# Performance work log

Hardware: AMD Instinct MI355X
Metric: run time of the kernel (lower is better)

The kernel has to match this reference:

```python
import jax, jax.numpy as jnp
import numpy as np

N = 20000      # nodes
E = 200000     # edges
F_IN = 512     # num_features
H = 1024       # hidden (hard-coded in module)
OUT = 128      # output_size


def setup_inputs() -> dict:
    key = jax.random.key(0)
    ks = jax.random.split(key, 12)
    x = jax.random.normal(ks[0], (N, F_IN), jnp.float32)
    edge_index = jax.random.randint(ks[1], (2, E), 0, N, dtype=jnp.int32)
    edge_weight = jax.random.uniform(ks[2], (E,), jnp.float32)
    # GCNConv weights (glorot-ish) and biases
    w1 = jax.random.normal(ks[3], (F_IN, H), jnp.float32) / np.sqrt(F_IN)
    b1 = jnp.zeros((H,), jnp.float32)
    w2 = jax.random.normal(ks[4], (H, OUT), jnp.float32) / np.sqrt(H)
    b2 = jnp.zeros((OUT,), jnp.float32)
    # residual Linear layers
    rw1 = jax.random.normal(ks[5], (F_IN, H), jnp.float32) / np.sqrt(F_IN)
    rb1 = jax.random.normal(ks[6], (H,), jnp.float32) * 0.01
    rw2 = jax.random.normal(ks[7], (H, OUT), jnp.float32) / np.sqrt(H)
    rb2 = jax.random.normal(ks[8], (OUT,), jnp.float32) * 0.01
    return {"x": x, "w1": w1, "b1": b1, "w2": w2, "b2": b2,
            "rw1": rw1, "rb1": rb1, "rw2": rw2, "rb2": rb2,
            "edge_weight": edge_weight, "edge_index": edge_index}


def gcn_conv(x, W, b, edge_index, edge_weight, n):
    """PyG GCNConv: linear transform, add self-loops (weight 1), sym-normalized scatter-add."""
    xw = x @ W                                             # [n, d_out]
    loop = jnp.arange(n, dtype=edge_index.dtype)
    row = jnp.concatenate([edge_index[0], loop])           # sources (x_j)
    col = jnp.concatenate([edge_index[1], loop])           # targets (aggregate here)
    ew = jnp.concatenate([edge_weight, jnp.ones((n,), xw.dtype)])
    deg = jax.ops.segment_sum(ew, col, num_segments=n)     # weighted in-degree
    dis = jnp.where(deg > 0, jax.lax.rsqrt(jnp.where(deg > 0, deg, 1.0)), 0.0)
    norm = dis[row] * ew * dis[col]                        # [E+n]
    msg = xw[row] * norm[:, None]                          # gather + scale
    out = jax.ops.segment_sum(msg, col, num_segments=n)    # scatter-add
    return out + b


def reference(x, w1, b1, w2, b2, rw1, rb1, rw2, rb2, edge_weight, edge_index):
    n = x.shape[0]
    h = jax.nn.relu(gcn_conv(x, w1, b1, edge_index, edge_weight, n) + (x @ rw1 + rb1))
    # F.dropout(training=False) is identity in eval mode
    out = gcn_conv(h, w2, b2, edge_index, edge_weight, n) + (h @ rw2 + rb2)
    return out
```

## Files before the change

kernel.cpp:

```cpp
#include <hip/hip_runtime.h>
#include <hip/hip_bf16.h>

#define NN 20000
#define EE 200000
#define FIN 512
#define HID 1024
#define OUTF 128
#define MPAD 20096

typedef unsigned short ush;
typedef __attribute__((ext_vector_type(8))) short bf16x8;
typedef __attribute__((ext_vector_type(4))) float f32x4;

__device__ __forceinline__ ush f2bf_rne(float f) {
    union { float f; unsigned u; } a; a.f = f;
    unsigned u = a.u;
    return (ush)((u + 0x7fffu + ((u >> 16) & 1u)) >> 16);
}
__device__ __forceinline__ float bf2f(ush h) {
    union { float f; unsigned u; } a; a.u = ((unsigned)h) << 16;
    return a.f;
}
__device__ __forceinline__ void split_bf(float v, ush& hi, ush& lo) {
    hi = f2bf_rne(v);
    lo = f2bf_rne(v - bf2f(hi));
}

__device__ __forceinline__ void gl16(const void* g, void* l) {
    __builtin_amdgcn_global_load_lds(
        (const __attribute__((address_space(1))) unsigned*)g,
        (__attribute__((address_space(3))) unsigned*)l, 16, 0, 0);
}

__global__ void init_kernel(float* deg, int* cnt, int n) {
    int i = blockIdx.x * blockDim.x + threadIdx.x;
    if (i < n) { deg[i] = 1.0f; cnt[i] = 0; }
}

__global__ void deg_count_kernel(const int* __restrict__ ei, const float* __restrict__ ew,
                                 float* deg, int* cnt, int e) {
    int idx = blockIdx.x * blockDim.x + threadIdx.x;
    if (idx < e) {
        int c = ei[EE + idx];
        atomicAdd(&deg[c], ew[idx]);
        atomicAdd(&cnt[c], 1);
    }
}

__global__ void dis_kernel(const float* __restrict__ deg, float* dis, int n) {
    int i = blockIdx.x * blockDim.x + threadIdx.x;
    if (i < n) dis[i] = rsqrtf(deg[i]);
}

__global__ void bias_kernel(const float* __restrict__ b1, const float* __restrict__ rb1,
                            const float* __restrict__ b2, const float* __restrict__ rb2,
                            float* bias1s, float* bias2s) {
    int i = blockIdx.x * blockDim.x + threadIdx.x;
    if (i < HID) bias1s[i] = b1[i] + rb1[i];
    if (i < OUTF) bias2s[i] = b2[i] + rb2[i];
}

#define SCAN_THREADS 1024
#define SCAN_CHUNK 20
__global__ __launch_bounds__(SCAN_THREADS)
void scan_kernel(const int* __restrict__ cnt, int* rowptr, int* cursor, int n, int total_e) {
    __shared__ int part[SCAN_THREADS];
    int t = threadIdx.x;
    int base = t * SCAN_CHUNK;
    int s = 0;
    for (int j = 0; j < SCAN_CHUNK; ++j) { int i = base + j; if (i < n) s += cnt[i]; }
    part[t] = s;
    __syncthreads();
    for (int off = 1; off < SCAN_THREADS; off <<= 1) {
        int add = (t >= off) ? part[t - off] : 0;
        __syncthreads();
        part[t] += add;
        __syncthreads();
    }
    int run = (t == 0) ? 0 : part[t - 1];
    for (int j = 0; j < SCAN_CHUNK; ++j) {
        int i = base + j;
        if (i < n) { rowptr[i] = run; cursor[i] = run; run += cnt[i]; }
    }
    if (t == SCAN_THREADS - 1) rowptr[n] = total_e;
}

__global__ void scatter_kernel(const int* __restrict__ ei, const float* __restrict__ ew,
                               const float* __restrict__ dis, int* cursor,
                               int* srcs, float* norms, int e) {
    int idx = blockIdx.x * blockDim.x + threadIdx.x;
    if (idx < e) {
        int r = ei[idx];
        int c = ei[EE + idx];
        float nv = dis[r] * ew[idx] * dis[c];
        int p = atomicAdd(&cursor[c], 1);
        srcs[p] = r;
        norms[p] = nv;
    }
}

__global__ void splitx_kernel(const float* __restrict__ x, ush* __restrict__ xh,
                              ush* __restrict__ xl) {
    int i = blockIdx.x * blockDim.x + threadIdx.x;
    if (i < NN * FIN / 4) {
        float4 v = ((const float4*)x)[i];
        ushort4 h, lo;
        split_bf(v.x, h.x, lo.x); split_bf(v.y, h.y, lo.y);
        split_bf(v.z, h.z, lo.z); split_bf(v.w, h.w, lo.w);
        ((ushort4*)xh)[i] = h;
        ((ushort4*)xl)[i] = lo;
    }
}

__global__ __launch_bounds__(256)
void tsplit_kernel(const float* __restrict__ src, int K, int N,
                   ush* __restrict__ dh, ush* __restrict__ dl, int ldst, int koff) {
    __shared__ float tile[32][33];
    int tx = threadIdx.x & 31, ty = threadIdx.x >> 5;
    int n0 = blockIdx.x * 32, k0 = blockIdx.y * 32;
#pragma unroll
    for (int i = 0; i < 4; ++i)
        tile[ty * 4 + i][tx] = src[(size_t)(k0 + ty * 4 + i) * N + n0 + tx];
    __syncthreads();
#pragma unroll
    for (int i = 0; i < 4; ++i) {
        int n = n0 + ty * 4 + i, k = k0 + tx;
        float v = tile[tx][ty * 4 + i];
        ush h, lo; split_bf(v, h, lo);
        size_t off = (size_t)n * ldst + koff + k;
        dh[off] = h;
        dl[off] = lo;
    }
}

__global__ __launch_bounds__(128)
void aggx_kernel(const float* __restrict__ x, ush* __restrict__ axh, ush* __restrict__ axl,
                 const float* __restrict__ dis,
                 const int* __restrict__ rowptr, const int* __restrict__ srcs,
                 const float* __restrict__ norms) {
    int i = blockIdx.x;
    int t = threadIdx.x;
    float d = dis[i];
    float d2 = d * d;
    float4 v = ((const float4*)(x + (size_t)i * FIN))[t];
    float s0 = d2 * v.x, s1 = d2 * v.y, s2 = d2 * v.z, s3 = d2 * v.w;
    int beg = rowptr[i], end = rowptr[i + 1];
    for (int j = beg; j < end; ++j) {
        int s = srcs[j];
        float w = norms[j];
        float4 u = ((const float4*)(x + (size_t)s * FIN))[t];
        s0 += w * u.x; s1 += w * u.y; s2 += w * u.z; s3 += w * u.w;
    }
    ushort4 hv, lv;
    split_bf(s0, hv.x, lv.x); split_bf(s1, hv.y, lv.y);
    split_bf(s2, hv.z, lv.z); split_bf(s3, hv.w, lv.w);
    ((ushort4*)(axh + (size_t)i * FIN))[t] = hv;
    ((ushort4*)(axl + (size_t)i * FIN))[t] = lv;
}

__global__ __launch_bounds__(256)
void gemm_mfma(const ush* __restrict__ A0h, const ush* __restrict__ A0l,
               const ush* __restrict__ A1h, const ush* __restrict__ A1l,
               int ksw, int KA,
               const ush* __restrict__ BTh0, const ush* __restrict__ BTl0,
               const ush* __restrict__ BTh1, const ush* __restrict__ BTl1,
               const float* __restrict__ bias0, const float* __restrict__ bias1,
               float* __restrict__ Cf0, float* __restrict__ Cf1,
               ush* __restrict__ Chh, ush* __restrict__ Chl,
               int M, int N, int K, int mode) {
    __shared__ ush Ah[128 * 32], Al[128 * 32], Bh[128 * 32], Bl[128 * 32];

    const ush* BTh = blockIdx.z ? BTh1 : BTh0;
    const ush* BTl = blockIdx.z ? BTl1 : BTl0;
    const float* bias = blockIdx.z ? bias1 : bias0;
    float* Cf = blockIdx.z ? Cf1 : Cf0;

    int t = threadIdx.x;
    int l = t & 63, w = t >> 6;
    int wr = w >> 1, wc = w & 1;
    int bm = blockIdx.x * 128, bn = blockIdx.y * 128;

    int sr = t >> 2;
    int sg8 = (t & 3) * 8;
    size_t a_off0 = (size_t)(bm + sr) * KA + sg8;
    size_t a_off1 = (size_t)(bm + 64 + sr) * KA + sg8;
    size_t b_off0 = (size_t)(bn + sr) * K + sg8;
    size_t b_off1 = (size_t)(bn + 64 + sr) * K + sg8;
    int lo0 = t * 16, lo1 = t * 16 + 4096;

    int abase = (wr * 64 + (l & 15)) * 64 + ((l >> 4) << 4);
    int bbase = (wc * 64 + (l & 15)) * 64 + ((l >> 4) << 4);

    f32x4 acc[4][4];
#pragma unroll
    for (int i = 0; i < 4; ++i)
#pragma unroll
        for (int j = 0; j < 4; ++j) acc[i][j] = (f32x4){0.f, 0.f, 0.f, 0.f};

    for (int kt = 0; kt < K; kt += 32) {
        const ush* Asrch; const ush* Asrcl; int kk;
        if (kt < ksw) { Asrch = A0h; Asrcl = A0l; kk = kt; }
        else          { Asrch = A1h; Asrcl = A1l; kk = kt - ksw; }

        gl16(Asrch + a_off0 + kk, (char*)Ah + lo0);
        gl16(Asrch + a_off1 + kk, (char*)Ah + lo1);
        gl16(Asrcl + a_off0 + kk, (char*)Al + lo0);
        gl16(Asrcl + a_off1 + kk, (char*)Al + lo1);
        gl16(BTh + b_off0 + kt, (char*)Bh + lo0);
        gl16(BTh + b_off1 + kt, (char*)Bh + lo1);
        gl16(BTl + b_off0 + kt, (char*)Bl + lo0);
        gl16(BTl + b_off1 + kt, (char*)Bl + lo1);
        __syncthreads();

        bf16x8 ah[4], al[4], bh[4], bl[4];
#pragma unroll
        for (int f = 0; f < 4; ++f) {
            ah[f] = *(const bf16x8*)((const char*)Ah + abase + f * 1024);
            al[f] = *(const bf16x8*)((const char*)Al + abase + f * 1024);
            bh[f] = *(const bf16x8*)((const char*)Bh + bbase + f * 1024);
            bl[f] = *(const bf16x8*)((const char*)Bl + bbase + f * 1024);
        }
#pragma unroll
        for (int fm = 0; fm < 4; ++fm)
#pragma unroll
            for (int fn = 0; fn < 4; ++fn)
                acc[fm][fn] = __builtin_amdgcn_mfma_f32_16x16x32_bf16(ah[fm], bh[fn], acc[fm][fn], 0, 0, 0);
#pragma unroll
        for (int fm = 0; fm < 4; ++fm)
#pragma unroll
            for (int fn = 0; fn < 4; ++fn)
                acc[fm][fn] = __builtin_amdgcn_mfma_f32_16x16x32_bf16(ah[fm], bl[fn], acc[fm][fn], 0, 0, 0);
#pragma unroll
        for (int fm = 0; fm < 4; ++fm)
#pragma unroll
            for (int fn = 0; fn < 4; ++fn)
                acc[fm][fn] = __builtin_amdgcn_mfma_f32_16x16x32_bf16(al[fm], bh[fn], acc[fm][fn], 0, 0, 0);
        __syncthreads();
    }

    int ccol = bn + wc * 64 + (l & 15);
    float bb[4];
#pragma unroll
    for (int fn = 0; fn < 4; ++fn) bb[fn] = bias ? bias[ccol + fn * 16] : 0.0f;

    if (mode) {
#pragma unroll
        for (int fm = 0; fm < 4; ++fm)
#pragma unroll
            for (int j = 0; j < 4; ++j) {
                int row = bm + wr * 64 + fm * 16 + ((l >> 4) << 2) + j;
                if (row < M) {
#pragma unroll
                    for (int fn = 0; fn < 4; ++fn) {
                        float v = fmaxf(acc[fm][fn][j] + bb[fn], 0.0f);
                        ush hi, lo; split_bf(v, hi, lo);
                        size_t off = (size_t)row * N + ccol + fn * 16;
                        Chh[off] = hi;
                        Chl[off] = lo;
                    }
                }
            }
    } else {
#pragma unroll
        for (int fm = 0; fm < 4; ++fm)
#pragma unroll
            for (int j = 0; j < 4; ++j) {
                int row = bm + wr * 64 + fm * 16 + ((l >> 4) << 2) + j;
                if (row < M) {
#pragma unroll
                    for (int fn = 0; fn < 4; ++fn)
                        Cf[(size_t)row * N + ccol + fn * 16] = acc[fm][fn][j] + bb[fn];
                }
            }
    }
}

__global__ __launch_bounds__(256)
void agg2_kernel(const float* __restrict__ xw, const float* __restrict__ res,
                 const float* __restrict__ dis,
                 const int* __restrict__ rowptr, const int* __restrict__ srcs,
                 const float* __restrict__ norms, float* __restrict__ out) {
    int wave = threadIdx.x >> 6;
    int lane = threadIdx.x & 63;
    int i = blockIdx.x * 4 + wave;
    float d = dis[i];
    float d2 = d * d;
    float2 v = ((const float2*)(xw + (size_t)i * OUTF))[lane];
    float ax = d2 * v.x, ay = d2 * v.y;
    int beg = rowptr[i], end = rowptr[i + 1];
    for (int j = beg; j < end; ++j) {
        int s = srcs[j];
        float w = norms[j];
        float2 u = ((const float2*)(xw + (size_t)s * OUTF))[lane];
        ax += w * u.x; ay += w * u.y;
    }
    float2 r = ((const float2*)(res + (size_t)i * OUTF))[lane];
    float2 o; o.x = ax + r.x; o.y = ay + r.y;
    ((float2*)(out + (size_t)i * OUTF))[lane] = o;
}

extern "C" void kernel_launch(void* const* d_in, const int* in_sizes, int n_in,
                              void* d_out, int out_size, void* d_ws, size_t ws_size,
                              hipStream_t stream) {
    const float* x   = (const float*)d_in[0];
    const float* w1  = (const float*)d_in[1];
    const float* b1  = (const float*)d_in[2];
    const float* w2  = (const float*)d_in[3];
    const float* b2  = (const float*)d_in[4];
    const float* rw1 = (const float*)d_in[5];
    const float* rb1 = (const float*)d_in[6];
    const float* rw2 = (const float*)d_in[7];
    const float* rb2 = (const float*)d_in[8];
    const float* ew  = (const float*)d_in[9];
    const int*   ei  = (const int*)d_in[10];
    float* out = (float*)d_out;

    char* p = (char*)d_ws;
    ush* xh  = (ush*)p; p += (size_t)MPAD * FIN * 2;
    ush* xl  = (ush*)p; p += (size_t)MPAD * FIN * 2;
    ush* axh = (ush*)p; p += (size_t)MPAD * FIN * 2;
    ush* axl = (ush*)p; p += (size_t)MPAD * FIN * 2;
    ush* hh  = (ush*)p; p += (size_t)MPAD * HID * 2;
    ush* hl  = (ush*)p; p += (size_t)MPAD * HID * 2;
    ush* w1cth = (ush*)p; p += (size_t)HID * HID * 2;
    ush* w1ctl = (ush*)p; p += (size_t)HID * HID * 2;
    ush* w2th  = (ush*)p; p += (size_t)OUTF * HID * 2;
    ush* w2tl  = (ush*)p; p += (size_t)OUTF * HID * 2;
    ush* rw2th = (ush*)p; p += (size_t)OUTF * HID * 2;
    ush* rw2tl = (ush*)p; p += (size_t)OUTF * HID * 2;
    float* deg    = (float*)p; p += NN * 4;
    float* dis    = (float*)p; p += NN * 4;
    float* norms  = (float*)p; p += EE * 4;
    float* bias1s = (float*)p; p += HID * 4;
    float* bias2s = (float*)p; p += OUTF * 4;
    int* rowptr = (int*)p; p += (NN + 1) * 4;
    int* cursor = (int*)p; p += NN * 4;
    int* cnt    = (int*)p; p += NN * 4;
    int* srcs   = (int*)p; p += EE * 4;
    float* xw2  = (float*)xh;
    float* res2 = (float*)xl;

    init_kernel<<<(NN + 255) / 256, 256, 0, stream>>>(deg, cnt, NN);
    deg_count_kernel<<<(EE + 255) / 256, 256, 0, stream>>>(ei, ew, deg, cnt, EE);
    dis_kernel<<<(NN + 255) / 256, 256, 0, stream>>>(deg, dis, NN);
    bias_kernel<<<(HID + 255) / 256, 256, 0, stream>>>(b1, rb1, b2, rb2, bias1s, bias2s);
    scan_kernel<<<1, SCAN_THREADS, 0, stream>>>(cnt, rowptr, cursor, NN, EE);
    scatter_kernel<<<(EE + 255) / 256, 256, 0, stream>>>(ei, ew, dis, cursor, srcs, norms, EE);

    splitx_kernel<<<(NN * FIN / 4 + 255) / 256, 256, 0, stream>>>(x, xh, xl);
    { dim3 g(HID / 32, FIN / 32); tsplit_kernel<<<g, 256, 0, stream>>>(w1,  FIN, HID, w1cth, w1ctl, HID, 0);   }
    { dim3 g(HID / 32, FIN / 32); tsplit_kernel<<<g, 256, 0, stream>>>(rw1, FIN, HID, w1cth, w1ctl, HID, FIN); }
    { dim3 g(OUTF / 32, HID / 32); tsplit_kernel<<<g, 256, 0, stream>>>(w2,  HID, OUTF, w2th,  w2tl,  HID, 0); }
    { dim3 g(OUTF / 32, HID / 32); tsplit_kernel<<<g, 256, 0, stream>>>(rw2, HID, OUTF, rw2th, rw2tl, HID, 0); }

    aggx_kernel<<<NN, 128, 0, stream>>>(x, axh, axl, dis, rowptr, srcs, norms);

    {
        dim3 grid(MPAD / 128, HID / 128, 1);
        gemm_mfma<<<grid, 256, 0, stream>>>(axh, axl, xh, xl, FIN, FIN,
                                            w1cth, w1ctl, w1cth, w1ctl,
                                            bias1s, bias1s,
                                            nullptr, nullptr, hh, hl,
                                            NN, HID, HID, 1);
    }
    {
        dim3 grid(MPAD / 128, OUTF / 128, 2);
        gemm_mfma<<<grid, 256, 0, stream>>>(hh, hl, hh, hl, HID, HID,
                                            w2th, w2tl, rw2th, rw2tl,
                                            nullptr, bias2s,
                                            xw2, res2, nullptr, nullptr,
                                            NN, OUTF, HID, 0);
    }
    agg2_kernel<<<NN / 4, 256, 0, stream>>>(xw2, res2, dis, rowptr, srcs, norms, out);
}
```

Baseline: 480.2 us.

## Fuse x split into aggregation, merge layer-2 GEMMs, swap grid order

```diff
diff --git a/kernel.cpp b/kernel.cpp
--- a/kernel.cpp
+++ b/kernel.cpp
@@ -54,10 +54,10 @@
 
 __global__ void bias_kernel(const float* __restrict__ b1, const float* __restrict__ rb1,
                             const float* __restrict__ b2, const float* __restrict__ rb2,
-                            float* bias1s, float* bias2s) {
+                            float* bias1s, float* bias2c) {
     int i = blockIdx.x * blockDim.x + threadIdx.x;
     if (i < HID) bias1s[i] = b1[i] + rb1[i];
-    if (i < OUTF) bias2s[i] = b2[i] + rb2[i];
+    if (i < 256) bias2c[i] = (i < 128) ? 0.0f : (b2[i - 128] + rb2[i - 128]);
 }
 
 #define SCAN_THREADS 1024
@@ -99,19 +99,6 @@
     }
 }
 
-__global__ void splitx_kernel(const float* __restrict__ x, ush* __restrict__ xh,
-                              ush* __restrict__ xl) {
-    int i = blockIdx.x * blockDim.x + threadIdx.x;
-    if (i < NN * FIN / 4) {
-        float4 v = ((const float4*)x)[i];
-        ushort4 h, lo;
-        split_bf(v.x, h.x, lo.x); split_bf(v.y, h.y, lo.y);
-        split_bf(v.z, h.z, lo.z); split_bf(v.w, h.w, lo.w);
-        ((ushort4*)xh)[i] = h;
-        ((ushort4*)xl)[i] = lo;
-    }
-}
-
 __global__ __launch_bounds__(256)
 void tsplit_kernel(const float* __restrict__ src, int K, int N,
                    ush* __restrict__ dh, ush* __restrict__ dl, int ldst, int koff) {
@@ -134,7 +121,9 @@
 }
 
 __global__ __launch_bounds__(128)
-void aggx_kernel(const float* __restrict__ x, ush* __restrict__ axh, ush* __restrict__ axl,
+void aggx_kernel(const float* __restrict__ x,
+                 ush* __restrict__ xh, ush* __restrict__ xl,
+                 ush* __restrict__ axh, ush* __restrict__ axl,
                  const float* __restrict__ dis,
                  const int* __restrict__ rowptr, const int* __restrict__ srcs,
                  const float* __restrict__ norms) {
@@ -143,13 +132,31 @@
     float d = dis[i];
     float d2 = d * d;
     float4 v = ((const float4*)(x + (size_t)i * FIN))[t];
+
+    ushort4 vh, vl;
+    split_bf(v.x, vh.x, vl.x); split_bf(v.y, vh.y, vl.y);
+    split_bf(v.z, vh.z, vl.z); split_bf(v.w, vh.w, vl.w);
+    ((ushort4*)(xh + (size_t)i * FIN))[t] = vh;
+    ((ushort4*)(xl + (size_t)i * FIN))[t] = vl;
+
     float s0 = d2 * v.x, s1 = d2 * v.y, s2 = d2 * v.z, s3 = d2 * v.w;
     int beg = rowptr[i], end = rowptr[i + 1];
-    for (int j = beg; j < end; ++j) {
-        int s = srcs[j];
-        float w = norms[j];
-        float4 u = ((const float4*)(x + (size_t)s * FIN))[t];
-        s0 += w * u.x; s1 += w * u.y; s2 += w * u.z; s3 += w * u.w;
+    int j = beg;
+    for (; j + 2 <= end; j += 2) {
+        int sa = srcs[j], sb = srcs[j + 1];
+        float wa = norms[j], wb = norms[j + 1];
+        float4 ua = ((const float4*)(x + (size_t)sa * FIN))[t];
+        float4 ub = ((const float4*)(x + (size_t)sb * FIN))[t];
+        s0 += wa * ua.x + wb * ub.x;
+        s1 += wa * ua.y + wb * ub.y;
+        s2 += wa * ua.z + wb * ub.z;
+        s3 += wa * ua.w + wb * ub.w;
+    }
+    if (j < end) {
+        int sa = srcs[j];
+        float wa = norms[j];
+        float4 ua = ((const float4*)(x + (size_t)sa * FIN))[t];
+        s0 += wa * ua.x; s1 += wa * ua.y; s2 += wa * ua.z; s3 += wa * ua.w;
     }
     ushort4 hv, lv;
     split_bf(s0, hv.x, lv.x); split_bf(s1, hv.y, lv.y);
@@ -162,23 +169,16 @@
 void gemm_mfma(const ush* __restrict__ A0h, const ush* __restrict__ A0l,
                const ush* __restrict__ A1h, const ush* __restrict__ A1l,
                int ksw, int KA,
-               const ush* __restrict__ BTh0, const ush* __restrict__ BTl0,
-               const ush* __restrict__ BTh1, const ush* __restrict__ BTl1,
-               const float* __restrict__ bias0, const float* __restrict__ bias1,
-               float* __restrict__ Cf0, float* __restrict__ Cf1,
-               ush* __restrict__ Chh, ush* __restrict__ Chl,
+               const ush* __restrict__ BTh, const ush* __restrict__ BTl,
+               const float* __restrict__ bias,
+               float* __restrict__ Cf, ush* __restrict__ Chh, ush* __restrict__ Chl,
                int M, int N, int K, int mode) {
     __shared__ ush Ah[128 * 32], Al[128 * 32], Bh[128 * 32], Bl[128 * 32];
-
-    const ush* BTh = blockIdx.z ? BTh1 : BTh0;
-    const ush* BTl = blockIdx.z ? BTl1 : BTl0;
-    const float* bias = blockIdx.z ? bias1 : bias0;
-    float* Cf = blockIdx.z ? Cf1 : Cf0;
 
     int t = threadIdx.x;
     int l = t & 63, w = t >> 6;
     int wr = w >> 1, wc = w & 1;
-    int bm = blockIdx.x * 128, bn = blockIdx.y * 128;
+    int bm = blockIdx.y * 128, bn = blockIdx.x * 128;
 
     int sr = t >> 2;
     int sg8 = (t & 3) * 8;
@@ -276,8 +276,7 @@
 }
 
 __global__ __launch_bounds__(256)
-void agg2_kernel(const float* __restrict__ xw, const float* __restrict__ res,
-                 const float* __restrict__ dis,
+void agg2_kernel(const float* __restrict__ z2, const float* __restrict__ dis,
                  const int* __restrict__ rowptr, const int* __restrict__ srcs,
                  const float* __restrict__ norms, float* __restrict__ out) {
     int wave = threadIdx.x >> 6;
@@ -285,16 +284,25 @@
     int i = blockIdx.x * 4 + wave;
     float d = dis[i];
     float d2 = d * d;
-    float2 v = ((const float2*)(xw + (size_t)i * OUTF))[lane];
+    float2 v = ((const float2*)(z2 + (size_t)i * 256))[lane];
     float ax = d2 * v.x, ay = d2 * v.y;
     int beg = rowptr[i], end = rowptr[i + 1];
-    for (int j = beg; j < end; ++j) {
-        int s = srcs[j];
-        float w = norms[j];
-        float2 u = ((const float2*)(xw + (size_t)s * OUTF))[lane];
-        ax += w * u.x; ay += w * u.y;
-    }
-    float2 r = ((const float2*)(res + (size_t)i * OUTF))[lane];
+    int j = beg;
+    for (; j + 2 <= end; j += 2) {
+        int sa = srcs[j], sb = srcs[j + 1];
+        float wa = norms[j], wb = norms[j + 1];
+        float2 ua = ((const float2*)(z2 + (size_t)sa * 256))[lane];
+        float2 ub = ((const float2*)(z2 + (size_t)sb * 256))[lane];
+        ax += wa * ua.x + wb * ub.x;
+        ay += wa * ua.y + wb * ub.y;
+    }
+    if (j < end) {
+        int sa = srcs[j];
+        float wa = norms[j];
+        float2 ua = ((const float2*)(z2 + (size_t)sa * 256))[lane];
+        ax += wa * ua.x; ay += wa * ua.y;
+    }
+    float2 r = ((const float2*)(z2 + (size_t)i * 256 + 128))[lane];
     float2 o; o.x = ax + r.x; o.y = ay + r.y;
     ((float2*)(out + (size_t)i * OUTF))[lane] = o;
 }
@@ -324,52 +332,47 @@
     ush* hl  = (ush*)p; p += (size_t)MPAD * HID * 2;
     ush* w1cth = (ush*)p; p += (size_t)HID * HID * 2;
     ush* w1ctl = (ush*)p; p += (size_t)HID * HID * 2;
-    ush* w2th  = (ush*)p; p += (size_t)OUTF * HID * 2;
-    ush* w2tl  = (ush*)p; p += (size_t)OUTF * HID * 2;
-    ush* rw2th = (ush*)p; p += (size_t)OUTF * HID * 2;
-    ush* rw2tl = (ush*)p; p += (size_t)OUTF * HID * 2;
+    ush* w2cth = (ush*)p; p += (size_t)256 * HID * 2;
+    ush* w2ctl = (ush*)p; p += (size_t)256 * HID * 2;
     float* deg    = (float*)p; p += NN * 4;
     float* dis    = (float*)p; p += NN * 4;
     float* norms  = (float*)p; p += EE * 4;
     float* bias1s = (float*)p; p += HID * 4;
-    float* bias2s = (float*)p; p += OUTF * 4;
+    float* bias2c = (float*)p; p += 256 * 4;
     int* rowptr = (int*)p; p += (NN + 1) * 4;
     int* cursor = (int*)p; p += NN * 4;
     int* cnt    = (int*)p; p += NN * 4;
     int* srcs   = (int*)p; p += EE * 4;
-    float* xw2  = (float*)xh;
-    float* res2 = (float*)xl;
+    float* z2 = (float*)xh;
 
     init_kernel<<<(NN + 255) / 256, 256, 0, stream>>>(deg, cnt, NN);
     deg_count_kernel<<<(EE + 255) / 256, 256, 0, stream>>>(ei, ew, deg, cnt, EE);
     dis_kernel<<<(NN + 255) / 256, 256, 0, stream>>>(deg, dis, NN);
-    bias_kernel<<<(HID + 255) / 256, 256, 0, stream>>>(b1, rb1, b2, rb2, bias1s, bias2s);
+    bias_kernel<<<(HID + 255) / 256, 256, 0, stream>>>(b1, rb1, b2, rb2, bias1s, bias2c);
     scan_kernel<<<1, SCAN_THREADS, 0, stream>>>(cnt, rowptr, cursor, NN, EE);
     scatter_kernel<<<(EE + 255) / 256, 256, 0, stream>>>(ei, ew, dis, cursor, srcs, norms, EE);
 
-    splitx_kernel<<<(NN * FIN / 4 + 255) / 256, 256, 0, stream>>>(x, xh, xl);
     { dim3 g(HID / 32, FIN / 32); tsplit_kernel<<<g, 256, 0, stream>>>(w1,  FIN, HID, w1cth, w1ctl, HID, 0);   }
     { dim3 g(HID / 32, FIN / 32); tsplit_kernel<<<g, 256, 0, stream>>>(rw1, FIN, HID, w1cth, w1ctl, HID, FIN); }
-    { dim3 g(OUTF / 32, HID / 32); tsplit_kernel<<<g, 256, 0, stream>>>(w2,  HID, OUTF, w2th,  w2tl,  HID, 0); }
-    { dim3 g(OUTF / 32, HID / 32); tsplit_kernel<<<g, 256, 0, stream>>>(rw2, HID, OUTF, rw2th, rw2tl, HID, 0); }
-
-    aggx_kernel<<<NN, 128, 0, stream>>>(x, axh, axl, dis, rowptr, srcs, norms);
+    { dim3 g(OUTF / 32, HID / 32); tsplit_kernel<<<g, 256, 0, stream>>>(w2,  HID, OUTF, w2cth, w2ctl, HID, 0); }
+    { dim3 g(OUTF / 32, HID / 32); tsplit_kernel<<<g, 256, 0, stream>>>(rw2, HID, OUTF,
+                                        w2cth + (size_t)128 * HID, w2ctl + (size_t)128 * HID, HID, 0); }
+
+    aggx_kernel<<<NN, 128, 0, stream>>>(x, xh, xl, axh, axl, dis, rowptr, srcs, norms);
 
     {
-        dim3 grid(MPAD / 128, HID / 128, 1);
+        dim3 grid(HID / 128, MPAD / 128);
         gemm_mfma<<<grid, 256, 0, stream>>>(axh, axl, xh, xl, FIN, FIN,
-                                            w1cth, w1ctl, w1cth, w1ctl,
-                                            bias1s, bias1s,
-                                            nullptr, nullptr, hh, hl,
+                                            w1cth, w1ctl, bias1s,
+                                            nullptr, hh, hl,
                                             NN, HID, HID, 1);
     }
     {
-        dim3 grid(MPAD / 128, OUTF / 128, 2);
+        dim3 grid(256 / 128, MPAD / 128);
         gemm_mfma<<<grid, 256, 0, stream>>>(hh, hl, hh, hl, HID, HID,
-                                            w2th, w2tl, rw2th, rw2tl,
-                                            nullptr, bias2s,
-                                            xw2, res2, nullptr, nullptr,
-                                            NN, OUTF, HID, 0);
-    }
-    agg2_kernel<<<NN / 4, 256, 0, stream>>>(xw2, res2, dis, rowptr, srcs, norms, out);
-}
+                                            w2cth, w2ctl, bias2c,
+                                            z2, nullptr, nullptr,
+                                            NN, 256, HID, 0);
+    }
+    agg2_kernel<<<NN / 4, 256, 0, stream>>>(z2, dis, rowptr, srcs, norms, out);
+}
```

Result: faster. 467.9 us (-2.6%).
